# Optimization experiments

Measured on AMD Instinct MI355X. Metric: run time of the kernel, lower is better.

## Reference

```python
import jax, jax.numpy as jnp
import numpy as np

K = 100
TEMPERATURE = 0.1


def setup_inputs() -> dict:
    key = jax.random.key(0)
    k1, k2 = jax.random.split(key)
    x = jax.random.normal(k1, (8, 128, 60, 60), dtype=jnp.float32)
    W = jax.random.normal(k2, (128, 2 * K), dtype=jnp.float32) * 0.02  # torch Linear(k*2, d_model).weight
    b = jnp.zeros((128,), dtype=jnp.float32)
    return {"x": x, "W": W, "b": b}


def reference(x, W, b):
    x0, x1 = jnp.split(x, 2, axis=0)
    n, c, h, w = x0.shape
    hw = h * w
    # n c h w -> n (h w) c
    f0 = jnp.transpose(x0.reshape(n, c, hw), (0, 2, 1))
    f1 = jnp.transpose(x1.reshape(n, c, hw), (0, 2, 1))
    # (f0/sqrt(c)) @ (f1/sqrt(c))^T / T  ==  f0 @ f1^T / (c*T)
    sm = jnp.einsum('nld,nsd->nls', f0, f1) / (c * TEMPERATURE)
    cm = (jax.nn.softmax(sm, axis=1) * jax.nn.softmax(sm, axis=2)).reshape(n, hw * hw)
    _, topi = jax.lax.top_k(cm, K)  # (n, K)
    qindex = topi // hw
    rindex = topi % hw
    coords0 = jnp.stack([qindex % w, qindex // w], axis=-1).astype(jnp.float32) / w  # (n, K, 2) as (x, y)
    coords1 = jnp.stack([rindex % w, rindex // w], axis=-1).astype(jnp.float32) / w
    # create_meshgrid(h, w, normalized=False): (1, h*w, 2) with (x, y), row-major
    gy, gx = jnp.meshgrid(jnp.arange(h), jnp.arange(w), indexing='ij')
    grid = jnp.stack([gx, gy], axis=-1).reshape(1, hw, 2).astype(jnp.float32) / w
    offsets0 = grid[:, :, None, :] - coords0[:, None, :, :]  # (n, hw, K, 2)
    offsets1 = grid[:, :, None, :] - coords1[:, None, :, :]
    emb0 = offsets0.reshape(n, hw, 2 * K) @ W.T + b  # (n, hw, d_model)
    emb1 = offsets1.reshape(n, hw, 2 * K) @ W.T + b
    f0 = f0 + emb0
    f1 = f1 + emb1
    f = jnp.concatenate([f0, f1], axis=0)  # (2n, hw, d)
    # n (h w) d -> n d h w
    return jnp.transpose(f, (0, 2, 1)).reshape(2 * n, c, h, w)
```

## Files before the change

kernel.cpp:

```cpp
#include <hip/hip_runtime.h>

#define HW 3600
#define PADR 3712
#define NF4 900
#define CAP 16384
#define KSEL 100
#define NT 58
typedef unsigned long long U64;

using short8   = __attribute__((ext_vector_type(8))) short;
using float4v  = __attribute__((ext_vector_type(4))) float;
using float16v = __attribute__((ext_vector_type(16))) float;

__device__ __forceinline__ unsigned monof(float f) {
    unsigned b = __float_as_uint(f);
    return (b & 0x80000000u) ? ~b : (b | 0x80000000u);
}
__device__ __forceinline__ float unmonof(unsigned m) {
    return __uint_as_float((m & 0x80000000u) ? (m ^ 0x80000000u) : ~m);
}
__device__ __forceinline__ unsigned short f2bf(float f) {
    unsigned b = __float_as_uint(f);
    return (unsigned short)((b + 0x7FFFu + ((b >> 16) & 1u)) >> 16);
}
__device__ __forceinline__ float bf2f(unsigned short h) {
    return __uint_as_float(((unsigned)h) << 16);
}
__device__ __forceinline__ void async16(const void* g, void* l) {
    __builtin_amdgcn_global_load_lds((const __attribute__((address_space(1))) void*)g,
                                     (__attribute__((address_space(3))) void*)l, 16, 0, 0);
}


__global__ __launch_bounds__(256) void conv_k(
    const float* __restrict__ x,
    unsigned short* __restrict__ hiT, unsigned short* __restrict__ loT,
    unsigned* __restrict__ zero_region)
{
    int b = blockIdx.z, l0 = blockIdx.x * 64, d0 = blockIdx.y * 64;
    __shared__ float t[64][65];
    int tid = threadIdx.x;
    if (blockIdx.y == 0 && blockIdx.z == 0) {
        int base = blockIdx.x * 512;
        for (int i = tid; i < 512; i += 256) {
            int g = base + i;
            if (g < 28808) zero_region[g] = 0u;
        }
    }
#pragma unroll
    for (int r = 0; r < 4; r++) {
        int idx = tid + 256 * r;
        int d = idx >> 4, lq = idx & 15;
        int l = l0 + lq * 4;
        const float* src = x + ((size_t)b * 128 + d0 + d) * HW;
        float4 v;
        if (l + 3 < HW) v = *(const float4*)(src + l);
        else {
            v.x = (l     < HW) ? src[l]     : 0.f;
            v.y = (l + 1 < HW) ? src[l + 1] : 0.f;
            v.z = (l + 2 < HW) ? src[l + 2] : 0.f;
            v.w = (l + 3 < HW) ? src[l + 3] : 0.f;
        }
        t[lq * 4 + 0][d] = v.x; t[lq * 4 + 1][d] = v.y;
        t[lq * 4 + 2][d] = v.z; t[lq * 4 + 3][d] = v.w;
    }
    __syncthreads();
    const int rblk = l0 >> 7;
#pragma unroll
    for (int r = 0; r < 2; r++) {
        int idx = tid + 256 * r;
        int l = idx & 63, dq = idx >> 6;
        unsigned hp[4], lp[4];
#pragma unroll
        for (int j = 0; j < 4; j++) {
            float f0 = t[l][dq * 8 + 2 * j], f1 = t[l][dq * 8 + 2 * j + 1];
            unsigned short h0 = f2bf(f0), h1 = f2bf(f1);
            unsigned short g0 = f2bf(f0 - bf2f(h0)), g1 = f2bf(f1 - bf2f(h1));
            hp[j] = (unsigned)h0 | ((unsigned)h1 << 16);
            lp[j] = (unsigned)g0 | ((unsigned)g1 << 16);
        }
        size_t o = ((size_t)(b * 29 + rblk) * 16 + (d0 >> 3) + dq) * 1024
                 + (size_t)((l0 + l) & 127) * 8;
        *(uint4*)(hiT + o) = make_uint4(hp[0], hp[1], hp[2], hp[3]);
        *(uint4*)(loT + o) = make_uint4(lp[0], lp[1], lp[2], lp[3]);
    }
}

__global__ __launch_bounds__(512) void gemm_mfma_k(
    const unsigned short* __restrict__ hiT, const unsigned short* __restrict__ loT,
    float* __restrict__ den_row, float* __restrict__ den_col,
    float* __restrict__ maxvt)
{
    const int batch = blockIdx.z, bx = blockIdx.x, by = blockIdx.y;
    __shared__ __align__(16) union SU {
        unsigned short st[2][4][4][128][8];
        struct {
            float rs[128];
            float cs[128];
            unsigned mx[256];
            float pad[7680];
            float T[8192];
        } ep;
    } u;

    const int tid = threadIdx.x;
    const int lane = tid & 63, w = tid >> 6;
    const int l31 = lane & 31, h = lane >> 5;
    const int p = w >> 1, halfr = w & 1;
    const int rg = w >> 2, cg = w & 3;

    const unsigned short* psrc = (p == 0) ? hiT : (p == 1) ? loT : (p == 2) ? hiT : loT;
    const int bsel = (p < 2) ? batch : batch + 4;
    const int rblk = (p < 2) ? by : bx;
    const size_t cbase = ((size_t)(bsel * 29 + rblk) * 16) * 1024;

    float16v acc[2];
    acc[0] = (float16v)(0.f);
    acc[1] = (float16v)(0.f);

#pragma unroll
    for (int kb = 0; kb < 4; kb++) {
        const unsigned short* g = psrc + cbase + (size_t)kb * 1024 + (halfr << 9) + lane * 8;
        async16(g, &u.st[0][p][kb][halfr << 6][0]);
    }

#pragma unroll
    for (int t = 0; t < 4; ++t) {
        const int cur = t & 1;
        __asm__ __volatile__("s_waitcnt vmcnt(0)" ::: "memory");
        __builtin_amdgcn_s_barrier();
        short8 fah[2][2], fal[2][2], fbh[2], fbl[2];
#pragma unroll
        for (int j = 0; j < 2; j++) {
            int kb = j * 2 + h;
            fah[j][0] = *(const short8*)&u.st[cur][0][kb][rg * 64 + l31][0];
            fah[j][1] = *(const short8*)&u.st[cur][0][kb][rg * 64 + 32 + l31][0];
            fal[j][0] = *(const short8*)&u.st[cur][1][kb][rg * 64 + l31][0];
            fal[j][1] = *(const short8*)&u.st[cur][1][kb][rg * 64 + 32 + l31][0];
            fbh[j]    = *(const short8*)&u.st[cur][2][kb][cg * 32 + l31][0];
            fbl[j]    = *(const short8*)&u.st[cur][3][kb][cg * 32 + l31][0];
        }
        if (t < 3) {
#pragma unroll
            for (int kb = 0; kb < 4; kb++) {
                const unsigned short* g = psrc + cbase + (size_t)((t + 1) * 4 + kb) * 1024
                                        + (halfr << 9) + lane * 8;
                async16(g, &u.st[cur ^ 1][p][kb][halfr << 6][0]);
            }
        }
        __builtin_amdgcn_sched_barrier(0);
#pragma unroll
        for (int j = 0; j < 2; j++) {
#pragma unroll
            for (int mt = 0; mt < 2; mt++) {
                acc[mt] = __builtin_amdgcn_mfma_f32_32x32x16_bf16(fah[j][mt], fbh[j], acc[mt], 0, 0, 0);
                acc[mt] = __builtin_amdgcn_mfma_f32_32x32x16_bf16(fah[j][mt], fbl[j], acc[mt], 0, 0, 0);
                acc[mt] = __builtin_amdgcn_mfma_f32_32x32x16_bf16(fal[j][mt], fbh[j], acc[mt], 0, 0, 0);
            }
        }
    }

    __builtin_amdgcn_s_barrier();
    if (tid < 128) { u.ep.rs[tid] = 0.f; u.ep.cs[tid] = 0.f; }
    if (tid < 256) u.ep.mx[tid] = 0u;
    __syncthreads();

    const float scale = 0.078125f;
    float* T = u.ep.T + w * 1024;
    const bool interior = (bx < 28) && (by < 28);
    const int col0 = bx * 128 + cg * 32 + l31;
    const bool cv = interior || (col0 < HW);
    float cs = 0.f;

#pragma unroll
    for (int mt = 0; mt < 2; mt++) {
#pragma unroll
        for (int reg = 0; reg < 16; reg++) {
            float v = acc[mt][reg] * scale;
            float e = cv ? __expf(v) : 0.f;
            int rloc = (reg & 3) + 8 * (reg >> 2) + 4 * h;
            bool rv = interior || (by * 128 + rg * 64 + mt * 32 + rloc < HW);
            if (rv) cs += e;
            T[rloc * 32 + (l31 ^ rloc)] = e;
        }
        __asm__ __volatile__("s_waitcnt lgkmcnt(0)" ::: "memory");
        {
            float ps = 0.f, pm = 0.f;
#pragma unroll
            for (int i = 0; i < 16; i++) {
                float tv_ = T[l31 * 32 + ((h * 16 + i) ^ l31)];
                ps += tv_;
                pm = fmaxf(pm, tv_);
            }
            ps += __shfl_xor(ps, 32);
            pm = fmaxf(pm, __shfl_xor(pm, 32));
            if (h == 0) {
                atomicAdd(&u.ep.rs[rg * 64 + mt * 32 + l31], ps);
                atomicMax(&u.ep.mx[(cg >> 1) * 128 + rg * 64 + mt * 32 + l31],
                          monof(__logf(pm)));
            }
        }
        __asm__ __volatile__("s_waitcnt lgkmcnt(0)" ::: "memory");
    }
    cs += __shfl_xor(cs, 32);
    if (h == 0) atomicAdd(&u.ep.cs[cg * 32 + l31], cs);
    __syncthreads();

    if (tid < 128) {
        int l = by * 128 + tid;
        if (l < HW) atomicAdd(&den_row[(size_t)batch * HW + l], u.ep.rs[tid]);
        int s = bx * 128 + tid;
        if (s < HW) atomicAdd(&den_col[(size_t)batch * HW + s], u.ep.cs[tid]);
    }
    if (tid < 256) {
        int tile = tid >> 7, row = tid & 127;
        int l = by * 128 + row;
        if (l < HW)
            maxvt[((size_t)batch * NT + bx * 2 + tile) * PADR + l] =
                unmonof(u.ep.mx[tile * 128 + row]);
    }
}

__global__ __launch_bounds__(256) void stat_k(
    const float* __restrict__ den_row, const float* __restrict__ den_col,
    const float* __restrict__ maxvt, float* __restrict__ keylb)
{
    const int b = blockIdx.z, tid = threadIdx.x;
    __shared__ float lncS[HW];
    __shared__ float mlsS[NT];
    for (int i = tid; i < HW; i += 256)
        lncS[i] = __logf(den_col[(size_t)b * HW + i]);
    __syncthreads();
    if (tid < NT) {
        float mx = -3.4e38f;
        int s0 = tid * 64, s1 = s0 + 64; if (s1 > HW) s1 = HW;
        for (int s = s0; s < s1; s++) mx = fmaxf(mx, lncS[s]);
        mlsS[tid] = (s0 < HW) ? mx : 1e30f;
    }
    __syncthreads();
    int j = blockIdx.x * 240 + tid;
    if (tid < 240 && j < HW) {
        const float* mvb = maxvt + (size_t)b * NT * PADR;
        float b0 = -3.4e38f, b1_ = -3.4e38f;
#pragma unroll 4
        for (int tt = 0; tt < 58; tt += 2) {
            b0  = fmaxf(b0,  2.0f * mvb[(size_t)tt * PADR + j]       - mlsS[tt]);
            b1_ = fmaxf(b1_, 2.0f * mvb[(size_t)(tt + 1) * PADR + j] - mlsS[tt + 1]);
        }
        keylb[(size_t)b * HW + j] = fmaxf(b0, b1_) - __logf(den_row[(size_t)b * HW + j]);
    }
}

__global__ __launch_bounds__(256) void tau_k(
    const float* __restrict__ keylb, float* __restrict__ tau)
{
    const int b = blockIdx.z, tid = threadIdx.x;
    __shared__ unsigned keyS[HW];
    __shared__ unsigned hist[4096];
    __shared__ unsigned hpc[256];
    __shared__ int b1S, c1S, b2S, lcnt;
    __shared__ unsigned bestS;
    __shared__ unsigned list[1024];

    for (int i = tid; i < 4096; i += 256) hist[i] = 0u;
    if (tid == 0) { lcnt = 0; bestS = 0u; }
    __syncthreads();
    for (int i = tid; i < HW; i += 256) {
        unsigned k = monof(keylb[(size_t)b * HW + i]);
        keyS[i] = k;
        atomicAdd(&hist[k >> 20], 1u);
    }
    __syncthreads();
    { unsigned s = 0; for (int j = 0; j < 16; j++) s += hist[tid * 16 + j]; hpc[tid] = s; }
    __syncthreads();
    if (tid == 0) {
        unsigned cum = 0; int cs_ = 255;
        for (; cs_ > 0; cs_--) { if (cum + hpc[cs_] >= (unsigned)KSEL) break; cum += hpc[cs_]; }
        int bb = cs_ * 16 + 15;
        for (; bb > cs_ * 16; bb--) { if (cum + hist[bb] >= (unsigned)KSEL) break; cum += hist[bb]; }
        b1S = bb; c1S = (int)cum;
    }
    __syncthreads();
    int b1 = b1S;
    for (int i = tid; i < 4096; i += 256) hist[i] = 0u;
    __syncthreads();
    for (int i = tid; i < HW; i += 256) {
        unsigned k = keyS[i];
        if ((int)(k >> 20) == b1) atomicAdd(&hist[(k >> 8) & 4095], 1u);
    }
    __syncthreads();
    { unsigned s = 0; for (int j = 0; j < 16; j++) s += hist[tid * 16 + j]; hpc[tid] = s; }
    __syncthreads();
    if (tid == 0) {
        unsigned cum = (unsigned)c1S; int cs_ = 255;
        for (; cs_ > 0; cs_--) { if (cum + hpc[cs_] >= (unsigned)KSEL) break; cum += hpc[cs_]; }
        int bb = cs_ * 16 + 15;
        for (; bb > cs_ * 16; bb--) { if (cum + hist[bb] >= (unsigned)KSEL) break; cum += hist[bb]; }
        b2S = bb;
    }
    __syncthreads();
    int b2 = b2S;
    for (int i = tid; i < HW; i += 256) {
        unsigned k = keyS[i]; int hb = (int)(k >> 20);
        if (hb > b1 || (hb == b1 && (int)((k >> 8) & 4095) >= b2)) {
            int p = atomicAdd(&lcnt, 1);
            if (p < 1024) list[p] = k;
        }
    }
    __syncthreads();
    int L = lcnt; if (L > 1024) L = 1024;
    for (int i = tid; i < L; i += 256) {
        unsigned e = list[i]; int c = 0;
        for (int j = 0; j < L; j++) c += (list[j] >= e) ? 1 : 0;
        if (c >= KSEL) atomicMax(&bestS, e);
    }
    __syncthreads();
    if (tid == 0) tau[b] = unmonof(bestS) - 3e-4f;
}

__global__ __launch_bounds__(256) void recollect_k(
    const unsigned short* __restrict__ hiT, const unsigned short* __restrict__ loT,
    const float* __restrict__ den_row, const float* __restrict__ den_col,
    const float* __restrict__ maxvt, const float* __restrict__ tau,
    uint2* __restrict__ cand, int* __restrict__ cnt)
{
    const int t = blockIdx.x, batch = blockIdx.y & 3, s = blockIdx.y >> 2;
    const int r0 = s * 900;
    const int tid = threadIdx.x;
    __shared__ float lnrS[900];
    __shared__ float lncS[64];
    __shared__ int prS[1024];
    __shared__ int pcS;
    __shared__ float mnlS;
    __shared__ __align__(16) unsigned short bS[2][16][64][8];

    const int lane = tid & 63, w = tid >> 6;
    const size_t bbase = (size_t)(batch + 4) * PADR * 128;

    {
        const size_t sbase = bbase + (size_t)(t >> 1) * 16 * 1024
                           + (size_t)(t & 1) * 512 + (size_t)lane * 8;
#pragma unroll
        for (int sl = w; sl < 32; sl += 4) {
            const int buf = sl >> 4, kb = sl & 15;
            const unsigned short* g = (buf ? loT : hiT) + sbase + (size_t)kb * 1024;
            async16(g, &bS[buf][kb][0][0]);
        }
    }

    if (tid < 64) {
        int c = t * 64 + tid;
        float lc = (c < HW) ? __logf(den_col[(size_t)batch * HW + c]) : 1e30f;
        lncS[tid] = lc;
        float mn = lc;
#pragma unroll
        for (int off = 1; off < 64; off <<= 1) mn = fminf(mn, __shfl_xor(mn, off));
        if (tid == 0) mnlS = mn;
    }
    for (int r = tid; r < 900; r += 256)
        lnrS[r] = __logf(den_row[(size_t)batch * HW + r0 + r]);
    if (tid == 0) pcS = 0;
    __syncthreads();

    const float tv = tau[batch];
    const float tvm = tv - 3e-4f;
    const float mnl = mnlS;
    const float* mv = maxvt + ((size_t)batch * NT + t) * PADR;
    for (int r = tid; r < 900; r += 256) {
        int rr = r0 + r;
        float bnd = 2.0f * mv[rr] - lnrS[r] - mnl;
        if (bnd >= tvm) {
            int p = atomicAdd(&pcS, 1);
            if (p < 1024) prS[p] = rr;
        }
    }
    __syncthreads();
    int pc = pcS; if (pc > 1024) pc = 1024;
    if (pc == 0) return;

    const int m = lane & 15, q = lane >> 4;
    const float scale = 0.078125f;
    const size_t abase = (size_t)batch * PADR * 128;

    for (int g = w; g * 16 < pc; g += 4) {
        int pi = g * 16 + m;
        int rowv = (pi < pc) ? prS[pi] : HW;
        float ldrv = (pi < pc) ? lnrS[rowv - r0] : 0.f;
        size_t arow = abase + ((size_t)(rowv >> 7) * 16) * 1024 + (size_t)(rowv & 127) * 8;

        float4v acc[4];
#pragma unroll
        for (int i = 0; i < 4; i++) acc[i] = (float4v){0.f, 0.f, 0.f, 0.f};
#pragma unroll
        for (int k0 = 0; k0 < 128; k0 += 32) {
            int kb = (k0 >> 3) + q;
            short8 ah = *(const short8*)(hiT + arow + (size_t)kb * 1024);
            short8 al = *(const short8*)(loT + arow + (size_t)kb * 1024);
#pragma unroll
            for (int nt = 0; nt < 4; nt++) {
                short8 bh = *(const short8*)&bS[0][kb][nt * 16 + m][0];
                short8 bl = *(const short8*)&bS[1][kb][nt * 16 + m][0];
                acc[nt] = __builtin_amdgcn_mfma_f32_16x16x32_bf16(ah, bh, acc[nt], 0, 0, 0);
                acc[nt] = __builtin_amdgcn_mfma_f32_16x16x32_bf16(ah, bl, acc[nt], 0, 0, 0);
                acc[nt] = __builtin_amdgcn_mfma_f32_16x16x32_bf16(al, bh, acc[nt], 0, 0, 0);
            }
        }
#pragma unroll
        for (int nt = 0; nt < 4; nt++) {
            int c = t * 64 + nt * 16 + m;
            if (c >= HW) continue;
            float ldc = lncS[nt * 16 + m];
#pragma unroll
            for (int r = 0; r < 4; r++) {
                int ri = q * 4 + r;
                if (g * 16 + ri >= pc) continue;
                int rowo = __shfl(rowv, ri);
                float ldro = __shfl(ldrv, ri);
                float v = acc[nt][r] * scale;
                float tt2 = 2.0f * v - ldro - ldc;
                if (tt2 >= tv) {
                    int p = atomicAdd(&cnt[batch], 1);
                    if (p < CAP)
                        cand[(size_t)batch * CAP + p] =
                            make_uint2(monof(tt2), (unsigned)(rowo * HW + c));
                }
            }
        }
    }
}

__global__ __launch_bounds__(1024) void select_k(
    const uint2* __restrict__ cand, const int* __restrict__ cnt,
    const float* __restrict__ W, const float* __restrict__ bias,
    float* __restrict__ cst, float* __restrict__ sxy)
{
    const int batch = blockIdx.x;
    const int tid = threadIdx.x;
    const uint2* cb = cand + (size_t)batch * CAP;
    __shared__ U64 lk[6144];
    __shared__ int topiS[KSEL];
    __shared__ float cqx[KSEL], cqy[KSEL], crx[KSEL], cry[KSEL];

    int M = cnt[batch]; if (M > CAP) M = CAP;
    const bool useL = (M <= 6144);
    if (useL)
        for (int i = tid; i < M; i += 1024) {
            uint2 e = cb[i];
            lk[i] = ((U64)e.x << 32) | (unsigned)(~e.y);
        }
    __syncthreads();
    for (int i = tid; i < M; i += 1024) {
        U64 e;
        if (useL) e = lk[i];
        else { uint2 tt = cb[i]; e = ((U64)tt.x << 32) | (unsigned)(~tt.y); }
        int r = 0;
        for (int j = 0; j < M; j++) {
            U64 o;
            if (useL) o = lk[j];
            else { uint2 tt = cb[j]; o = ((U64)tt.x << 32) | (unsigned)(~tt.y); }
            r += (o > e) ? 1 : 0;
        }
        if (r < KSEL) topiS[r] = (int)(~(unsigned)(e & 0xffffffffu));
    }
    __syncthreads();
    if (tid < KSEL) {
        int idx = topiS[tid];
        int qq = idx / HW, rr = idx - qq * HW;
        cqx[tid] = (float)(qq % 60) / 60.0f;
        cqy[tid] = (float)(qq / 60) / 60.0f;
        crx[tid] = (float)(rr % 60) / 60.0f;
        cry[tid] = (float)(rr / 60) / 60.0f;
    }
    __syncthreads();
    if (tid < 256) {
        const int d = tid & 127, hf = tid >> 7;
        const float* wrow = W + d * 200;
        float sx = 0.f, sy = 0.f, c = 0.f;
#pragma unroll 4
        for (int k = 0; k < KSEL; k++) {
            float wx = wrow[2 * k], wy = wrow[2 * k + 1];
            sx += wx; sy += wy;
            float cx = hf ? crx[k] : cqx[k];
            float cy = hf ? cry[k] : cqy[k];
            c += cx * wx + cy * wy;
        }
        cst[(hf ? (batch + 4) : batch) * 128 + d] = bias[d] - c;
        if (batch == 0 && hf == 0) { sxy[d] = sx; sxy[128 + d] = sy; }
    }
}

__global__ __launch_bounds__(256) void final_k(
    const float* __restrict__ x, const float* __restrict__ cst,
    const float* __restrict__ sxy, float* __restrict__ out)
{
    const int bd = blockIdx.x;
    const int d = bd & 127;
    const int tid = threadIdx.x;
    const float cstv = cst[bd];
    const float sx = sxy[d], sy = sxy[128 + d];
    const float4* xin = (const float4*)(x + (size_t)bd * HW);
    float4* o4 = (float4*)(out + (size_t)bd * HW);
    for (int f = tid; f < NF4; f += 256) {
        float4 v = xin[f];
        int p0 = f * 4;
        float gy = (float)(p0 / 60) / 60.0f;
        float gxb = (float)(p0 % 60);
        float add = cstv + gy * sy;
        v.x += add + ((gxb      ) / 60.0f) * sx;
        v.y += add + ((gxb + 1.f) / 60.0f) * sx;
        v.z += add + ((gxb + 2.f) / 60.0f) * sx;
        v.w += add + ((gxb + 3.f) / 60.0f) * sx;
        o4[f] = v;
    }
}

extern "C" void kernel_launch(void* const* d_in, const int* in_sizes, int n_in,
                              void* d_out, int out_size, void* d_ws, size_t ws_size,
                              hipStream_t stream)
{
    const float* x    = (const float*)d_in[0];
    const float* W    = (const float*)d_in[1];
    const float* bias = (const float*)d_in[2];
    float* out = (float*)d_out;

    char* ws = (char*)d_ws;
    float*    den_row = (float*)(ws + 0);
    float*    den_col = (float*)(ws + 57600);
    int*      cnt     = (int*)  (ws + 115200);
    float*    tau     = (float*)(ws + 115216);
    float*    keylb   = (float*)(ws + 115264);
    float*    cst     = (float*)(ws + 115264);
    float*    sxy     = (float*)(ws + 119360);
    uint2*    cand    = (uint2*)(ws + 172864);
    float*    maxvt   = (float*)(ws + 697152);
    unsigned short* hiT = (unsigned short*)(ws + 4141888);
    unsigned short* loT = (unsigned short*)(ws + 11744064);

    conv_k     <<<dim3(58, 2, 8),  256, 0, stream>>>(x, hiT, loT, (unsigned*)ws);
    gemm_mfma_k<<<dim3(29, 29, 4), 512, 0, stream>>>(hiT, loT, den_row, den_col, maxvt);
    stat_k     <<<dim3(15, 1, 4),  256, 0, stream>>>(den_row, den_col, maxvt, keylb);
    tau_k      <<<dim3(1, 1, 4),   256, 0, stream>>>(keylb, tau);
    recollect_k<<<dim3(NT, 16),    256, 0, stream>>>(hiT, loT, den_row, den_col, maxvt, tau, cand, cnt);
    select_k   <<<dim3(4),         1024, 0, stream>>>(cand, cnt, W, bias, cst, sxy);
    final_k    <<<dim3(1024),      256, 0, stream>>>(x, cst, sxy, out);
}
```

Before: 224.7 us.

## Load GEMM fragments directly from global, remap blocks per XCD, radix-select top-k

The GEMM kernel no longer stages operands through double-buffered LDS with async copies. Each wave now loads its MFMA fragments straight from global memory. Block indices are remapped so that neighbouring tiles land on the same XCD, and launch bounds now request higher occupancy. The select kernel replaces an O(M^2) rank sort over all candidates with a two-pass 12-bit radix histogram that finds the top-100 threshold, then ranks only a short list of at most 1024 survivors. This cuts select cost sharply but may drop correct results if more than 1024 candidates tie at the threshold, and direct global loads may hurt GEMM reuse.

```diff
diff --git a/kernel.cpp b/kernel.cpp
--- a/kernel.cpp
+++ b/kernel.cpp
@@ -86,69 +86,55 @@
     }
 }
 
-__global__ __launch_bounds__(512) void gemm_mfma_k(
+__global__ __launch_bounds__(512, 4) void gemm_mfma_k(
     const unsigned short* __restrict__ hiT, const unsigned short* __restrict__ loT,
     float* __restrict__ den_row, float* __restrict__ den_col,
     float* __restrict__ maxvt)
 {
-    const int batch = blockIdx.z, bx = blockIdx.x, by = blockIdx.y;
-    __shared__ __align__(16) union SU {
-        unsigned short st[2][4][4][128][8];
-        struct {
-            float rs[128];
-            float cs[128];
-            unsigned mx[256];
-            float pad[7680];
-            float T[8192];
-        } ep;
-    } u;
+    const int nwg = 29 * 29 * 4, q = nwg >> 3, r = nwg & 7;
+    int orig = blockIdx.x + 29 * (blockIdx.y + 29 * blockIdx.z);
+    int xcd = orig & 7, idx = orig >> 3;
+    int wg = (xcd < r ? xcd * (q + 1) : r * (q + 1) + (xcd - r) * q) + idx;
+    const int bx = wg % 29; int tmp = wg / 29;
+    const int by = tmp % 29; const int batch = tmp / 29;
+
+    __shared__ float T[8][1024];
+    __shared__ float rsB[128];
+    __shared__ float csB[128];
+    __shared__ unsigned mxB[2][128];
 
     const int tid = threadIdx.x;
     const int lane = tid & 63, w = tid >> 6;
     const int l31 = lane & 31, h = lane >> 5;
-    const int p = w >> 1, halfr = w & 1;
     const int rg = w >> 2, cg = w & 3;
 
-    const unsigned short* psrc = (p == 0) ? hiT : (p == 1) ? loT : (p == 2) ? hiT : loT;
-    const int bsel = (p < 2) ? batch : batch + 4;
-    const int rblk = (p < 2) ? by : bx;
-    const size_t cbase = ((size_t)(bsel * 29 + rblk) * 16) * 1024;
+    if (tid < 128) { rsB[tid] = 0.f; csB[tid] = 0.f; }
+    if (tid < 256) mxB[tid >> 7][tid & 127] = 0u;
+
+    const size_t cbaseA = ((size_t)(batch * 29 + by) * 16) * 1024;
+    const size_t cbaseB = ((size_t)((batch + 4) * 29 + bx) * 16) * 1024;
+    const unsigned short* Ah = hiT + cbaseA + (size_t)h * 1024 + (size_t)(rg * 64 + l31) * 8;
+    const unsigned short* Al = loT + cbaseA + (size_t)h * 1024 + (size_t)(rg * 64 + l31) * 8;
+    const unsigned short* Bh = hiT + cbaseB + (size_t)h * 1024 + (size_t)(cg * 32 + l31) * 8;
+    const unsigned short* Bl = loT + cbaseB + (size_t)h * 1024 + (size_t)(cg * 32 + l31) * 8;
 
     float16v acc[2];
     acc[0] = (float16v)(0.f);
     acc[1] = (float16v)(0.f);
 
 #pragma unroll
-    for (int kb = 0; kb < 4; kb++) {
-        const unsigned short* g = psrc + cbase + (size_t)kb * 1024 + (halfr << 9) + lane * 8;
-        async16(g, &u.st[0][p][kb][halfr << 6][0]);
-    }
-
-#pragma unroll
-    for (int t = 0; t < 4; ++t) {
-        const int cur = t & 1;
-        __asm__ __volatile__("s_waitcnt vmcnt(0)" ::: "memory");
-        __builtin_amdgcn_s_barrier();
+    for (int ks = 0; ks < 4; ks++) {
         short8 fah[2][2], fal[2][2], fbh[2], fbl[2];
 #pragma unroll
         for (int j = 0; j < 2; j++) {
-            int kb = j * 2 + h;
-            fah[j][0] = *(const short8*)&u.st[cur][0][kb][rg * 64 + l31][0];
-            fah[j][1] = *(const short8*)&u.st[cur][0][kb][rg * 64 + 32 + l31][0];
-            fal[j][0] = *(const short8*)&u.st[cur][1][kb][rg * 64 + l31][0];
-            fal[j][1] = *(const short8*)&u.st[cur][1][kb][rg * 64 + 32 + l31][0];
-            fbh[j]    = *(const short8*)&u.st[cur][2][kb][cg * 32 + l31][0];
-            fbl[j]    = *(const short8*)&u.st[cur][3][kb][cg * 32 + l31][0];
-        }
-        if (t < 3) {
-#pragma unroll
-            for (int kb = 0; kb < 4; kb++) {
-                const unsigned short* g = psrc + cbase + (size_t)((t + 1) * 4 + kb) * 1024
-                                        + (halfr << 9) + lane * 8;
-                async16(g, &u.st[cur ^ 1][p][kb][halfr << 6][0]);
-            }
-        }
-        __builtin_amdgcn_sched_barrier(0);
+            const size_t off = (size_t)(ks * 4 + j * 2) * 1024;
+            fah[j][0] = *(const short8*)(Ah + off);
+            fah[j][1] = *(const short8*)(Ah + off + 256);
+            fal[j][0] = *(const short8*)(Al + off);
+            fal[j][1] = *(const short8*)(Al + off + 256);
+            fbh[j]    = *(const short8*)(Bh + off);
+            fbl[j]    = *(const short8*)(Bl + off);
+        }
 #pragma unroll
         for (int j = 0; j < 2; j++) {
 #pragma unroll
@@ -159,14 +145,10 @@
             }
         }
     }
-
-    __builtin_amdgcn_s_barrier();
-    if (tid < 128) { u.ep.rs[tid] = 0.f; u.ep.cs[tid] = 0.f; }
-    if (tid < 256) u.ep.mx[tid] = 0u;
     __syncthreads();
 
     const float scale = 0.078125f;
-    float* T = u.ep.T + w * 1024;
+    float* Tw = &T[w][0];
     const bool interior = (bx < 28) && (by < 28);
     const int col0 = bx * 128 + cg * 32 + l31;
     const bool cv = interior || (col0 < HW);
@@ -181,43 +163,43 @@
             int rloc = (reg & 3) + 8 * (reg >> 2) + 4 * h;
             bool rv = interior || (by * 128 + rg * 64 + mt * 32 + rloc < HW);
             if (rv) cs += e;
-            T[rloc * 32 + (l31 ^ rloc)] = e;
+            Tw[rloc * 32 + (l31 ^ rloc)] = e;
         }
         __asm__ __volatile__("s_waitcnt lgkmcnt(0)" ::: "memory");
         {
             float ps = 0.f, pm = 0.f;
 #pragma unroll
             for (int i = 0; i < 16; i++) {
-                float tv_ = T[l31 * 32 + ((h * 16 + i) ^ l31)];
+                float tv_ = Tw[l31 * 32 + ((h * 16 + i) ^ l31)];
                 ps += tv_;
                 pm = fmaxf(pm, tv_);
             }
             ps += __shfl_xor(ps, 32);
             pm = fmaxf(pm, __shfl_xor(pm, 32));
             if (h == 0) {
-                atomicAdd(&u.ep.rs[rg * 64 + mt * 32 + l31], ps);
-                atomicMax(&u.ep.mx[(cg >> 1) * 128 + rg * 64 + mt * 32 + l31],
+                atomicAdd(&rsB[rg * 64 + mt * 32 + l31], ps);
+                atomicMax(&mxB[cg >> 1][rg * 64 + mt * 32 + l31],
                           monof(__logf(pm)));
             }
         }
         __asm__ __volatile__("s_waitcnt lgkmcnt(0)" ::: "memory");
     }
     cs += __shfl_xor(cs, 32);
-    if (h == 0) atomicAdd(&u.ep.cs[cg * 32 + l31], cs);
+    if (h == 0) atomicAdd(&csB[cg * 32 + l31], cs);
     __syncthreads();
 
     if (tid < 128) {
         int l = by * 128 + tid;
-        if (l < HW) atomicAdd(&den_row[(size_t)batch * HW + l], u.ep.rs[tid]);
+        if (l < HW) atomicAdd(&den_row[(size_t)batch * HW + l], rsB[tid]);
         int s = bx * 128 + tid;
-        if (s < HW) atomicAdd(&den_col[(size_t)batch * HW + s], u.ep.cs[tid]);
+        if (s < HW) atomicAdd(&den_col[(size_t)batch * HW + s], csB[tid]);
     }
     if (tid < 256) {
         int tile = tid >> 7, row = tid & 127;
         int l = by * 128 + row;
         if (l < HW)
             maxvt[((size_t)batch * NT + bx * 2 + tile) * PADR + l] =
-                unmonof(u.ep.mx[tile * 128 + row]);
+                unmonof(mxB[tile][row]);
     }
 }
 
@@ -437,29 +419,61 @@
     const int batch = blockIdx.x;
     const int tid = threadIdx.x;
     const uint2* cb = cand + (size_t)batch * CAP;
-    __shared__ U64 lk[6144];
+    __shared__ unsigned hist[4096];
+    __shared__ unsigned hpc[256];
+    __shared__ int b1S, c1S, b2S, lcnt;
+    __shared__ U64 list[1024];
     __shared__ int topiS[KSEL];
     __shared__ float cqx[KSEL], cqy[KSEL], crx[KSEL], cry[KSEL];
 
     int M = cnt[batch]; if (M > CAP) M = CAP;
-    const bool useL = (M <= 6144);
-    if (useL)
-        for (int i = tid; i < M; i += 1024) {
-            uint2 e = cb[i];
-            lk[i] = ((U64)e.x << 32) | (unsigned)(~e.y);
-        }
+    for (int i = tid; i < 4096; i += 1024) hist[i] = 0u;
+    if (tid == 0) lcnt = 0;
+    __syncthreads();
+    for (int i = tid; i < M; i += 1024) atomicAdd(&hist[cb[i].x >> 20], 1u);
+    __syncthreads();
+    if (tid < 256) { unsigned s = 0; for (int j = 0; j < 16; j++) s += hist[tid * 16 + j]; hpc[tid] = s; }
+    __syncthreads();
+    if (tid == 0) {
+        unsigned cum = 0; int cs_ = 255;
+        for (; cs_ > 0; cs_--) { if (cum + hpc[cs_] >= (unsigned)KSEL) break; cum += hpc[cs_]; }
+        int bb = cs_ * 16 + 15;
+        for (; bb > cs_ * 16; bb--) { if (cum + hist[bb] >= (unsigned)KSEL) break; cum += hist[bb]; }
+        b1S = bb; c1S = (int)cum;
+    }
+    __syncthreads();
+    const int b1 = b1S;
+    for (int i = tid; i < 4096; i += 1024) hist[i] = 0u;
     __syncthreads();
     for (int i = tid; i < M; i += 1024) {
-        U64 e;
-        if (useL) e = lk[i];
-        else { uint2 tt = cb[i]; e = ((U64)tt.x << 32) | (unsigned)(~tt.y); }
-        int r = 0;
-        for (int j = 0; j < M; j++) {
-            U64 o;
-            if (useL) o = lk[j];
-            else { uint2 tt = cb[j]; o = ((U64)tt.x << 32) | (unsigned)(~tt.y); }
-            r += (o > e) ? 1 : 0;
-        }
+        unsigned x = cb[i].x;
+        if ((int)(x >> 20) == b1) atomicAdd(&hist[(x >> 8) & 4095], 1u);
+    }
+    __syncthreads();
+    if (tid < 256) { unsigned s = 0; for (int j = 0; j < 16; j++) s += hist[tid * 16 + j]; hpc[tid] = s; }
+    __syncthreads();
+    if (tid == 0) {
+        unsigned cum = (unsigned)c1S; int cs_ = 255;
+        for (; cs_ > 0; cs_--) { if (cum + hpc[cs_] >= (unsigned)KSEL) break; cum += hpc[cs_]; }
+        int bb = cs_ * 16 + 15;
+        for (; bb > cs_ * 16; bb--) { if (cum + hist[bb] >= (unsigned)KSEL) break; cum += hist[bb]; }
+        b2S = bb;
+    }
+    __syncthreads();
+    const int b2 = b2S;
+    for (int i = tid; i < M; i += 1024) {
+        uint2 e = cb[i];
+        int hb = (int)(e.x >> 20);
+        if (hb > b1 || (hb == b1 && (int)((e.x >> 8) & 4095) >= b2)) {
+            int p = atomicAdd(&lcnt, 1);
+            if (p < 1024) list[p] = ((U64)e.x << 32) | (unsigned)(~e.y);
+        }
+    }
+    __syncthreads();
+    int L = lcnt; if (L > 1024) L = 1024;
+    for (int i = tid; i < L; i += 1024) {
+        U64 e = list[i]; int r = 0;
+        for (int j = 0; j < L; j++) r += (list[j] > e) ? 1 : 0;
         if (r < KSEL) topiS[r] = (int)(~(unsigned)(e & 0xffffffffu));
     }
     __syncthreads();
```

Measured after the change: 226.7 us. No clear change (+0.9%).
